# Performance work log

Hardware: AMD Instinct MI355X
Metric: run time of the kernel (lower is better)

Reference implementation:

```python
import jax, jax.numpy as jnp
import numpy as np

D_IN = 1024
D_OUT = 1024
NUM_HEADS = 16
HEAD_DIM = D_OUT // NUM_HEADS


def setup_inputs() -> dict:
    key = jax.random.key(0)
    kx, kq, kk, kv, ko = jax.random.split(key, 5)
    s = 1.0 / np.sqrt(D_IN)
    return {
        "x": jax.random.normal(kx, (1, 4096, D_IN), dtype=jnp.float32),
        "Wq": jax.random.normal(kq, (D_IN, D_OUT), dtype=jnp.float32) * s,
        "Wk": jax.random.normal(kk, (D_IN, D_OUT), dtype=jnp.float32) * s,
        "Wv": jax.random.normal(kv, (D_IN, D_OUT), dtype=jnp.float32) * s,
        "Wo": jax.random.normal(ko, (D_OUT, D_OUT), dtype=jnp.float32) * s,
    }


def reference(x, Wq, Wk, Wv, Wo):
    b, s, _ = x.shape
    # project and split heads: [b, h, s, d]
    def split_heads(t):
        return t.reshape(b, s, NUM_HEADS, HEAD_DIM).transpose(0, 2, 1, 3)
    Q = split_heads(x @ Wq)
    K = split_heads(x @ Wk)
    V = split_heads(x @ Wv)
    scores = jnp.einsum("bhqd,bhkd->bhqk", Q, K) / jnp.sqrt(jnp.float32(HEAD_DIM))
    causal = jnp.triu(jnp.ones((s, s), dtype=bool), k=1)  # True above diagonal
    scores = jnp.where(causal, -jnp.inf, scores)
    probs = jax.nn.softmax(scores, axis=-1)
    out = jnp.einsum("bhqk,bhkd->bhqd", probs, V)
    out = out.transpose(0, 2, 1, 3).reshape(b, s, D_OUT)
    return out @ Wo
```

## Files before the change

kernel.cpp:

```cpp
#include <hip/hip_runtime.h>
#include <cstdint>

#define S_LEN 4096
#define D_MODEL 1024
#define NHEAD 16
#define HDIM 64

typedef __bf16 bf16_t;
typedef __bf16 bf16x8 __attribute__((ext_vector_type(8)));
typedef __bf16 bf16x4 __attribute__((ext_vector_type(4)));
typedef float floatx4 __attribute__((ext_vector_type(4)));

#define QSCALE 0.18033688011112042f

__device__ __forceinline__ void lds_cp16(void* lds, const void* g) {
    __builtin_amdgcn_global_load_lds(
        (const __attribute__((address_space(1))) unsigned int*)g,
        (__attribute__((address_space(3))) unsigned int*)lds,
        16, 0, 0);
}

__device__ __forceinline__ float fast_exp2(float x) {
    float r;
    asm("v_exp_f32 %0, %1" : "=v"(r) : "v"(x));
    return r;
}

__global__ __launch_bounds__(256) void k_prep(const float* __restrict__ x,
                                              const float* __restrict__ Wq,
                                              const float* __restrict__ Wk,
                                              const float* __restrict__ Wv,
                                              const float* __restrict__ Wo,
                                              bf16_t* __restrict__ xb,
                                              bf16_t* __restrict__ WtQKV,
                                              bf16_t* __restrict__ WtO) {
    const int bx = blockIdx.x;
    if (bx < 4096) {
        int i = bx * 256 + threadIdx.x;
        float4 v = ((const float4*)x)[i];
        bf16x4 o;
        o[0] = (bf16_t)v.x; o[1] = (bf16_t)v.y; o[2] = (bf16_t)v.z; o[3] = (bf16_t)v.w;
        *(bf16x4*)(xb + (size_t)i * 4) = o;
        return;
    }
    __shared__ float lds[64][65];
    const int i = bx - 4096;
    const int z = i >> 8, rem = i & 255;
    const float* W = (z == 0) ? Wq : (z == 1) ? Wk : (z == 2) ? Wv : Wo;
    bf16_t* Wt = (z < 3) ? (WtQKV + (size_t)z * 1048576) : WtO;
    const int k0 = (rem >> 4) * 64, n0 = (rem & 15) * 64;
    const int t = threadIdx.x, cl = t & 63, rl = t >> 6;
#pragma unroll
    for (int r = 0; r < 16; ++r)
        lds[r * 4 + rl][cl] = W[(size_t)(k0 + r * 4 + rl) * 1024 + n0 + cl];
    __syncthreads();
#pragma unroll
    for (int r = 0; r < 16; ++r)
        Wt[(size_t)(n0 + r * 4 + rl) * 1024 + k0 + cl] = (bf16_t)lds[cl][r * 4 + rl];
}

template <int MODE, int MT>
__global__ __launch_bounds__(256) void k_gemm(const bf16_t* __restrict__ A,
                                              const bf16_t* __restrict__ Bt,
                                              float* __restrict__ Cout,
                                              bf16_t* __restrict__ Qb,
                                              bf16_t* __restrict__ Kb,
                                              bf16_t* __restrict__ Vt,
                                              const bf16_t* __restrict__ OP1x,
                                              const float* __restrict__ Lpx) {
    constexpr int MI = MT / 32;
    constexpr int GX = 4096 / MT;
    constexpr int GY = (MODE == 1) ? 24 : 8;
    constexpr int NWG = GX * GY;
    __shared__ __align__(16) bf16_t sA[MT * 32];
    __shared__ __align__(16) bf16_t sB[128 * 32];
    const int t = threadIdx.x, w = t >> 6, lane = t & 63, quad = lane >> 4, l15 = lane & 15;
    int lin = (int)blockIdx.y * GX + (int)blockIdx.x;
    lin = (lin & 7) * (NWG / 8) + (lin >> 3);
    const int bxr = lin % GX, byr = lin / GX;
    const int m0 = bxr * MT, n0 = byr * 128;
    const int wm = w >> 1, wn = w & 1;

    floatx4 acc[MI][4];
#pragma unroll
    for (int i = 0; i < MI; ++i)
#pragma unroll
        for (int j = 0; j < 4; ++j)
            acc[i][j] = floatx4{0.f, 0.f, 0.f, 0.f};

    const int crow = m0 + (t >> 2), ckq = t & 3;
    bf16x8 cA{}, cB{};
    float cla = 0.f, clb = 0.f;
    if (MODE == 2) {
        cA = *(const bf16x8*)(A + (size_t)crow * 1024 + ckq * 8);
        cB = *(const bf16x8*)(OP1x + (size_t)crow * 1024 + ckq * 8);
        cla = Lpx[crow];
        clb = Lpx[65536 + crow];
    }

    for (int kb = 0; kb < 32; ++kb) {
        __syncthreads();
        if (MODE == 2) {
            float inv = __builtin_amdgcn_rcpf(cla + clb);
            bf16x8 o;
#pragma unroll
            for (int e = 0; e < 8; ++e)
                o[e] = (bf16_t)(((float)cA[e] + (float)cB[e]) * inv);
            *(bf16x8*)&sA[t * 8] = o;
            if (kb + 1 < 32) {
                int h2 = (kb + 1) >> 1;
                int col = (kb + 1) * 32 + ckq * 8;
                cA = *(const bf16x8*)(A + (size_t)crow * 1024 + col);
                cB = *(const bf16x8*)(OP1x + (size_t)crow * 1024 + col);
                cla = Lpx[h2 * 4096 + crow];
                clb = Lpx[65536 + h2 * 4096 + crow];
            }
        } else {
#pragma unroll
            for (int r = 0; r < MT / 64; ++r) {
                int c = t + 256 * r;
                int row = c >> 2, kq = c & 3;
                lds_cp16(&sA[w * 512 + r * 2048],
                         A + (size_t)(m0 + row) * 1024 + kb * 32 + kq * 8);
            }
        }
#pragma unroll
        for (int r = 0; r < 2; ++r) {
            int c = t + 256 * r;
            int row = c >> 2, kq = c & 3;
            lds_cp16(&sB[w * 512 + r * 2048],
                     Bt + (size_t)(n0 + row) * 1024 + kb * 32 + kq * 8);
        }
        __syncthreads();
        bf16x8 af[MI], bfr[4];
#pragma unroll
        for (int i = 0; i < MI; ++i)
            af[i] = *(const bf16x8*)&sA[(wm * (MT / 2) + i * 16 + l15) * 32 + quad * 8];
#pragma unroll
        for (int j = 0; j < 4; ++j)
            bfr[j] = *(const bf16x8*)&sB[(wn * 64 + j * 16 + l15) * 32 + quad * 8];
#pragma unroll
        for (int i = 0; i < MI; ++i)
#pragma unroll
            for (int j = 0; j < 4; ++j)
                acc[i][j] = __builtin_amdgcn_mfma_f32_16x16x32_bf16(af[i], bfr[j],
                                                                    acc[i][j], 0, 0, 0);
    }

    const int mrow = m0 + wm * (MT / 2) + quad * 4;
    if (MODE == 0 || MODE == 2) {
        const int ncol = n0 + wn * 64 + l15;
#pragma unroll
        for (int i = 0; i < MI; ++i)
#pragma unroll
            for (int j = 0; j < 4; ++j)
#pragma unroll
                for (int r = 0; r < 4; ++r)
                    Cout[(size_t)(mrow + i * 16 + r) * 1024 + ncol + j * 16] = acc[i][j][r];
    } else {
        const int g = byr >> 3;
        const int ncbase = (byr & 7) * 128 + wn * 64 + l15;
        if (g == 2) {
#pragma unroll
            for (int j = 0; j < 4; ++j) {
                int nc = ncbase + j * 16;
                int hh = nc >> 6, dd = nc & 63;
                bf16_t* dst = Vt + (size_t)hh * 262144 + (size_t)dd * 64;
#pragma unroll
                for (int i = 0; i < MI; ++i) {
                    int s0r = mrow + i * 16;
                    bf16x4 pk;
                    pk[0] = (bf16_t)acc[i][j][0]; pk[1] = (bf16_t)acc[i][j][1];
                    pk[2] = (bf16_t)acc[i][j][2]; pk[3] = (bf16_t)acc[i][j][3];
                    int kk = s0r & 63;
                    int pp = (kk & 0x20) | ((kk & 0xC) << 1) | ((kk & 0x10) >> 2);
                    *(bf16x4*)&dst[(size_t)(s0r >> 6) * 4096 + pp] = pk;
                }
            }
        } else {
            bf16_t* base = g ? Kb : Qb;
            const float sc = g ? 1.0f : QSCALE;
#pragma unroll
            for (int j = 0; j < 4; ++j) {
                int nc = ncbase + j * 16;
                int hh = nc >> 6, dd = nc & 63;
#pragma unroll
                for (int i = 0; i < MI; ++i)
#pragma unroll
                    for (int r = 0; r < 4; ++r)
                        base[(size_t)hh * 262144 + (size_t)(mrow + i * 16 + r) * 64 + dd] =
                            (bf16_t)(acc[i][j][r] * sc);
            }
        }
    }
}

__global__ __launch_bounds__(256, 4) void k_attn(const bf16_t* __restrict__ Qb,
                                                 const bf16_t* __restrict__ Kb,
                                                 const bf16_t* __restrict__ Vt,
                                                 bf16_t* __restrict__ OP0,
                                                 bf16_t* __restrict__ OP1,
                                                 float* __restrict__ Lp) {
    __shared__ __align__(16) bf16_t Ks[2][64 * 64];
    __shared__ __align__(16) bf16_t Vts[2][64 * 64];
    const int bid = blockIdx.x;
    const int slot = bid >> 8, jj = bid & 255, g = jj >> 5, u = jj & 31;
    const int h = u >> 1, sp = u & 1;
    const int qb = (slot == 0) ? (31 - g) : (slot == 1) ? (16 + g)
                 : (slot == 2) ? (15 - g) : g;
    const int t = threadIdx.x, w = t >> 6, quad = (t & 63) >> 4, l15 = t & 15;
    const bf16_t* Qh = Qb + (size_t)h * 262144;
    const bf16_t* Kh = Kb + (size_t)h * 262144;
    const bf16_t* Vth = Vt + (size_t)h * 262144;

    const bf16_t* Qrow = Qh + (size_t)(qb * 128 + w * 32 + l15) * 64;
    bf16x8 bq[2][2];
#pragma unroll
    for (int qt = 0; qt < 2; ++qt)
#pragma unroll
        for (int kh = 0; kh < 2; ++kh)
            bq[qt][kh] = *(const bf16x8*)(Qrow + qt * 1024 + kh * 32 + quad * 8);

    bf16x8 vones;
#pragma unroll
    for (int e = 0; e < 8; ++e) vones[e] = (bf16_t)1.0f;

    floatx4 lacc[2];
    floatx4 o_acc[2][4];
#pragma unroll
    for (int qt = 0; qt < 2; ++qt) {
        lacc[qt] = floatx4{0.f, 0.f, 0.f, 0.f};
#pragma unroll
        for (int j = 0; j < 4; ++j) o_acc[qt][j] = floatx4{0.f, 0.f, 0.f, 0.f};
    }

#define STAGE_K(b, kb_)                                                            \
    {                                                                              \
        _Pragma("unroll") for (int r = 0; r < 2; ++r) {                            \
            int c = t + 256 * r;                                                   \
            int row = c >> 3, sw = (c & 7) ^ (row & 7);                            \
            lds_cp16(&Ks[b][c * 8], Kh + (size_t)(kb_) * 4096 + row * 64 + sw * 8);\
        }                                                                          \
    }
#define STAGE_V(b, kb_)                                                            \
    {                                                                              \
        _Pragma("unroll") for (int r = 0; r < 2; ++r) {                            \
            int c = t + 256 * r;                                                   \
            int row = c >> 3, sw = (c & 7) ^ (row & 7);                            \
            lds_cp16(&Vts[b][c * 8], Vth + (size_t)(kb_) * 4096 + row * 64 + sw * 8);\
        }                                                                          \
    }

    const int t0 = sp ? (qb + 1) : 0;
    const int nIter = qb + 1;
    const int qmax = qb * 128 + w * 32 + 31;

    STAGE_K(0, t0)
    STAGE_V(0, t0)
    for (int it = 0; it < nIter; ++it) {
        const int kb = t0 + it;
        const int buf = it & 1;
        __syncthreads();
        if (it + 1 < nIter) {
            STAGE_K(buf ^ 1, kb + 1)
            STAGE_V(buf ^ 1, kb + 1)
        }
        const bool active = (kb * 64 <= qmax);

        if (active) {
            floatx4 st[2][4];
            __builtin_amdgcn_s_setprio(1);
#pragma unroll
            for (int j = 0; j < 4; ++j) {
                int rk = j * 16 + l15;
                bf16x8 a0 = *(const bf16x8*)&Ks[buf][rk * 64 + ((quad ^ (rk & 7)) * 8)];
                bf16x8 a1 = *(const bf16x8*)&Ks[buf][rk * 64 + (((quad + 4) ^ (rk & 7)) * 8)];
#pragma unroll
                for (int qt = 0; qt < 2; ++qt) {
                    floatx4 z = {0.f, 0.f, 0.f, 0.f};
                    st[qt][j] = __builtin_amdgcn_mfma_f32_16x16x32_bf16(a0, bq[qt][0], z, 0, 0, 0);
                    st[qt][j] = __builtin_amdgcn_mfma_f32_16x16x32_bf16(a1, bq[qt][1], st[qt][j], 0, 0, 0);
                }
            }
            __builtin_amdgcn_s_setprio(0);
            if (kb >= 2 * qb) {
#pragma unroll
                for (int qt = 0; qt < 2; ++qt) {
                    int qg = qb * 128 + w * 32 + qt * 16 + l15;
#pragma unroll
                    for (int j = 0; j < 4; ++j)
#pragma unroll
                        for (int r = 0; r < 4; ++r) {
                            int keyg = kb * 64 + j * 16 + quad * 4 + r;
                            if (keyg > qg) st[qt][j][r] = -1e30f;
                        }
                }
            }
            bf16x8 pa[2][2];
#pragma unroll
            for (int qt = 0; qt < 2; ++qt) {
#pragma unroll
                for (int j = 0; j < 4; ++j) {
                    st[qt][j][0] = fast_exp2(st[qt][j][0]);
                    st[qt][j][1] = fast_exp2(st[qt][j][1]);
                    st[qt][j][2] = fast_exp2(st[qt][j][2]);
                    st[qt][j][3] = fast_exp2(st[qt][j][3]);
                }
#pragma unroll
                for (int kh = 0; kh < 2; ++kh)
#pragma unroll
                    for (int m = 0; m < 4; ++m) {
                        pa[qt][kh][m]     = (bf16_t)st[qt][2 * kh][m];
                        pa[qt][kh][4 + m] = (bf16_t)st[qt][2 * kh + 1][m];
                    }
            }
            __builtin_amdgcn_s_setprio(1);
#pragma unroll
            for (int kh = 0; kh < 2; ++kh) {
                int pc = kh * 4 + quad;
#pragma unroll
                for (int j = 0; j < 4; ++j) {
                    int rd = j * 16 + l15;
                    bf16x8 bv = *(const bf16x8*)&Vts[buf][rd * 64 + ((pc ^ (rd & 7)) * 8)];
                    o_acc[0][j] = __builtin_amdgcn_mfma_f32_16x16x32_bf16(pa[0][kh], bv, o_acc[0][j], 0, 0, 0);
                    o_acc[1][j] = __builtin_amdgcn_mfma_f32_16x16x32_bf16(pa[1][kh], bv, o_acc[1][j], 0, 0, 0);
                }
                lacc[0] = __builtin_amdgcn_mfma_f32_16x16x32_bf16(pa[0][kh], vones, lacc[0], 0, 0, 0);
                lacc[1] = __builtin_amdgcn_mfma_f32_16x16x32_bf16(pa[1][kh], vones, lacc[1], 0, 0, 0);
            }
            __builtin_amdgcn_s_setprio(0);
        }
    }
    bf16_t* OPx = sp ? OP1 : OP0;
#pragma unroll
    for (int qt = 0; qt < 2; ++qt) {
        if (l15 == 0)
            *(floatx4*)&Lp[sp * 65536 + h * 4096 + qb * 128 + w * 32 + qt * 16 + quad * 4] =
                lacc[qt];
#pragma unroll
        for (int r = 0; r < 4; ++r) {
            int rowg = qb * 128 + w * 32 + qt * 16 + quad * 4 + r;
#pragma unroll
            for (int j = 0; j < 4; ++j)
                OPx[(size_t)rowg * 1024 + h * 64 + j * 16 + l15] = (bf16_t)o_acc[qt][j][r];
        }
    }
#undef STAGE_K
#undef STAGE_V
}

extern "C" void kernel_launch(void* const* d_in, const int* in_sizes, int n_in,
                              void* d_out, int out_size, void* d_ws, size_t ws_size,
                              hipStream_t stream) {
    const float* x  = (const float*)d_in[0];
    const float* Wq = (const float*)d_in[1];
    const float* Wk = (const float*)d_in[2];
    const float* Wv = (const float*)d_in[3];
    const float* Wo = (const float*)d_in[4];

    bf16_t* ws = (bf16_t*)d_ws;
    bf16_t* Xb    = ws;
    bf16_t* WtQKV = Xb + 4194304;
    bf16_t* WtO   = WtQKV + 3145728;
    bf16_t* Qb    = WtO + 1048576;
    bf16_t* Kb    = Qb + 4194304;
    bf16_t* Vt    = Kb + 4194304;
    bf16_t* OP1   = Vt + 4194304;
    bf16_t* OP0   = Xb;
    float*  Lp    = (float*)WtQKV;
    float* out = (float*)d_out;

    k_prep<<<5120, 256, 0, stream>>>(x, Wq, Wk, Wv, Wo, Xb, WtQKV, WtO);
    k_gemm<1, 128><<<dim3(32, 24), 256, 0, stream>>>(Xb, WtQKV, nullptr, Qb, Kb, Vt,
                                                     nullptr, nullptr);
    k_attn<<<1024, 256, 0, stream>>>(Qb, Kb, Vt, OP0, OP1, Lp);
    k_gemm<2, 64><<<dim3(64, 8), 256, 0, stream>>>(OP0, WtO, out, nullptr, nullptr,
                                                   nullptr, OP1, Lp);
}
```

Before: 192.8 us.

## Use persistent atomic work queue with 3-way KV split for long attention rows

The attention kernel becomes persistent. Each block grabs chunks from a global atomic counter that is zeroed in the prep kernel and stored in the output buffer. The upper half of query blocks now splits the KV range three ways instead of two, with a third partial output buffer OP2. The output GEMM merges three partial sums for those rows. The aim is better load balance on the causal triangle; the cost is atomic overhead, extra partial-output traffic, and removal of the GEMM block-swizzle remapping.

```diff
diff --git a/kernel.cpp b/kernel.cpp
--- a/kernel.cpp
+++ b/kernel.cpp
@@ -12,6 +12,7 @@
 typedef float floatx4 __attribute__((ext_vector_type(4)));
 
 #define QSCALE 0.18033688011112042f
+#define NCHUNK 1280
 
 __device__ __forceinline__ void lds_cp16(void* lds, const void* g) {
     __builtin_amdgcn_global_load_lds(
@@ -33,7 +34,8 @@
                                               const float* __restrict__ Wo,
                                               bf16_t* __restrict__ xb,
                                               bf16_t* __restrict__ WtQKV,
-                                              bf16_t* __restrict__ WtO) {
+                                              bf16_t* __restrict__ WtO,
+                                              unsigned int* __restrict__ ctr) {
     const int bx = blockIdx.x;
     if (bx < 4096) {
         int i = bx * 256 + threadIdx.x;
@@ -43,6 +45,7 @@
         *(bf16x4*)(xb + (size_t)i * 4) = o;
         return;
     }
+    if (bx == 4096 && threadIdx.x == 0) *ctr = 0u;
     __shared__ float lds[64][65];
     const int i = bx - 4096;
     const int z = i >> 8, rem = i & 255;
@@ -67,18 +70,13 @@
                                               bf16_t* __restrict__ Kb,
                                               bf16_t* __restrict__ Vt,
                                               const bf16_t* __restrict__ OP1x,
+                                              const bf16_t* __restrict__ OP2x,
                                               const float* __restrict__ Lpx) {
     constexpr int MI = MT / 32;
-    constexpr int GX = 4096 / MT;
-    constexpr int GY = (MODE == 1) ? 24 : 8;
-    constexpr int NWG = GX * GY;
     __shared__ __align__(16) bf16_t sA[MT * 32];
     __shared__ __align__(16) bf16_t sB[128 * 32];
     const int t = threadIdx.x, w = t >> 6, lane = t & 63, quad = lane >> 4, l15 = lane & 15;
-    int lin = (int)blockIdx.y * GX + (int)blockIdx.x;
-    lin = (lin & 7) * (NWG / 8) + (lin >> 3);
-    const int bxr = lin % GX, byr = lin / GX;
-    const int m0 = bxr * MT, n0 = byr * 128;
+    const int m0 = blockIdx.x * MT, n0 = blockIdx.y * 128;
     const int wm = w >> 1, wn = w & 1;
 
     floatx4 acc[MI][4];
@@ -89,23 +87,28 @@
             acc[i][j] = floatx4{0.f, 0.f, 0.f, 0.f};
 
     const int crow = m0 + (t >> 2), ckq = t & 3;
-    bf16x8 cA{}, cB{};
-    float cla = 0.f, clb = 0.f;
+    const bool hasC = (MODE == 2) && (crow >= 2048);
+    bf16x8 cA{}, cB{}, cC{};
+    float cla = 0.f, clb = 0.f, clc = 0.f;
     if (MODE == 2) {
         cA = *(const bf16x8*)(A + (size_t)crow * 1024 + ckq * 8);
         cB = *(const bf16x8*)(OP1x + (size_t)crow * 1024 + ckq * 8);
         cla = Lpx[crow];
         clb = Lpx[65536 + crow];
+        if (hasC) {
+            cC = *(const bf16x8*)(OP2x + (size_t)(crow - 2048) * 1024 + ckq * 8);
+            clc = Lpx[131072 + crow];
+        }
     }
 
     for (int kb = 0; kb < 32; ++kb) {
         __syncthreads();
         if (MODE == 2) {
-            float inv = __builtin_amdgcn_rcpf(cla + clb);
+            float inv = __builtin_amdgcn_rcpf(cla + clb + clc);
             bf16x8 o;
 #pragma unroll
             for (int e = 0; e < 8; ++e)
-                o[e] = (bf16_t)(((float)cA[e] + (float)cB[e]) * inv);
+                o[e] = (bf16_t)(((float)cA[e] + (float)cB[e] + (float)cC[e]) * inv);
             *(bf16x8*)&sA[t * 8] = o;
             if (kb + 1 < 32) {
                 int h2 = (kb + 1) >> 1;
@@ -114,6 +117,10 @@
                 cB = *(const bf16x8*)(OP1x + (size_t)crow * 1024 + col);
                 cla = Lpx[h2 * 4096 + crow];
                 clb = Lpx[65536 + h2 * 4096 + crow];
+                if (hasC) {
+                    cC = *(const bf16x8*)(OP2x + (size_t)(crow - 2048) * 1024 + col);
+                    clc = Lpx[131072 + h2 * 4096 + crow];
+                }
             }
         } else {
 #pragma unroll
@@ -158,8 +165,8 @@
                 for (int r = 0; r < 4; ++r)
                     Cout[(size_t)(mrow + i * 16 + r) * 1024 + ncol + j * 16] = acc[i][j][r];
     } else {
-        const int g = byr >> 3;
-        const int ncbase = (byr & 7) * 128 + wn * 64 + l15;
+        const int g = (int)blockIdx.y >> 3;
+        const int ncbase = ((int)blockIdx.y & 7) * 128 + wn * 64 + l15;
         if (g == 2) {
 #pragma unroll
             for (int j = 0; j < 4; ++j) {
@@ -200,39 +207,17 @@
                                                  const bf16_t* __restrict__ Vt,
                                                  bf16_t* __restrict__ OP0,
                                                  bf16_t* __restrict__ OP1,
-                                                 float* __restrict__ Lp) {
+                                                 bf16_t* __restrict__ OP2,
+                                                 float* __restrict__ Lp,
+                                                 unsigned int* __restrict__ ctr) {
     __shared__ __align__(16) bf16_t Ks[2][64 * 64];
     __shared__ __align__(16) bf16_t Vts[2][64 * 64];
-    const int bid = blockIdx.x;
-    const int slot = bid >> 8, jj = bid & 255, g = jj >> 5, u = jj & 31;
-    const int h = u >> 1, sp = u & 1;
-    const int qb = (slot == 0) ? (31 - g) : (slot == 1) ? (16 + g)
-                 : (slot == 2) ? (15 - g) : g;
+    __shared__ int sid;
     const int t = threadIdx.x, w = t >> 6, quad = (t & 63) >> 4, l15 = t & 15;
-    const bf16_t* Qh = Qb + (size_t)h * 262144;
-    const bf16_t* Kh = Kb + (size_t)h * 262144;
-    const bf16_t* Vth = Vt + (size_t)h * 262144;
-
-    const bf16_t* Qrow = Qh + (size_t)(qb * 128 + w * 32 + l15) * 64;
-    bf16x8 bq[2][2];
-#pragma unroll
-    for (int qt = 0; qt < 2; ++qt)
-#pragma unroll
-        for (int kh = 0; kh < 2; ++kh)
-            bq[qt][kh] = *(const bf16x8*)(Qrow + qt * 1024 + kh * 32 + quad * 8);
 
     bf16x8 vones;
 #pragma unroll
     for (int e = 0; e < 8; ++e) vones[e] = (bf16_t)1.0f;
-
-    floatx4 lacc[2];
-    floatx4 o_acc[2][4];
-#pragma unroll
-    for (int qt = 0; qt < 2; ++qt) {
-        lacc[qt] = floatx4{0.f, 0.f, 0.f, 0.f};
-#pragma unroll
-        for (int j = 0; j < 4; ++j) o_acc[qt][j] = floatx4{0.f, 0.f, 0.f, 0.f};
-    }
 
 #define STAGE_K(b, kb_)                                                            \
     {                                                                              \
@@ -251,98 +236,144 @@
         }                                                                          \
     }
 
-    const int t0 = sp ? (qb + 1) : 0;
-    const int nIter = qb + 1;
-    const int qmax = qb * 128 + w * 32 + 31;
-
-    STAGE_K(0, t0)
-    STAGE_V(0, t0)
-    for (int it = 0; it < nIter; ++it) {
-        const int kb = t0 + it;
-        const int buf = it & 1;
+    for (;;) {
+        if (t == 0) sid = (int)atomicAdd(ctr, 1u);
         __syncthreads();
-        if (it + 1 < nIter) {
-            STAGE_K(buf ^ 1, kb + 1)
-            STAGE_V(buf ^ 1, kb + 1)
-        }
-        const bool active = (kb * 64 <= qmax);
-
-        if (active) {
-            floatx4 st[2][4];
-            __builtin_amdgcn_s_setprio(1);
-#pragma unroll
-            for (int j = 0; j < 4; ++j) {
-                int rk = j * 16 + l15;
-                bf16x8 a0 = *(const bf16x8*)&Ks[buf][rk * 64 + ((quad ^ (rk & 7)) * 8)];
-                bf16x8 a1 = *(const bf16x8*)&Ks[buf][rk * 64 + (((quad + 4) ^ (rk & 7)) * 8)];
+        const int id = sid;
+        if (id >= NCHUNK) break;
+
+        int qb, h, part, c0, c1;
+        if (id < 768) {
+            qb = 31 - id / 48;
+            int r = id % 48;
+            h = r / 3; part = r % 3;
+            int L = 2 * qb + 2, base = L / 3, rem = L % 3;
+            int mn = part < rem ? part : rem;
+            c0 = part * base + mn;
+            c1 = c0 + base + (part < rem ? 1 : 0);
+        } else {
+            int j = id - 768;
+            qb = 15 - (j >> 5);
+            int r = j & 31;
+            h = r >> 1; part = r & 1;
+            c0 = part ? (qb + 1) : 0;
+            c1 = part ? (2 * qb + 2) : (qb + 1);
+        }
+        const bf16_t* Qh = Qb + (size_t)h * 262144;
+        const bf16_t* Kh = Kb + (size_t)h * 262144;
+        const bf16_t* Vth = Vt + (size_t)h * 262144;
+
+        const bf16_t* Qrow = Qh + (size_t)(qb * 128 + w * 32 + l15) * 64;
+        bf16x8 bq[2][2];
+#pragma unroll
+        for (int qt = 0; qt < 2; ++qt)
+#pragma unroll
+            for (int kh = 0; kh < 2; ++kh)
+                bq[qt][kh] = *(const bf16x8*)(Qrow + qt * 1024 + kh * 32 + quad * 8);
+
+        floatx4 lacc[2];
+        floatx4 o_acc[2][4];
+#pragma unroll
+        for (int qt = 0; qt < 2; ++qt) {
+            lacc[qt] = floatx4{0.f, 0.f, 0.f, 0.f};
+#pragma unroll
+            for (int j = 0; j < 4; ++j) o_acc[qt][j] = floatx4{0.f, 0.f, 0.f, 0.f};
+        }
+
+        const int nIter = c1 - c0;
+        const int qmax = qb * 128 + w * 32 + 31;
+
+        STAGE_K(0, c0)
+        STAGE_V(0, c0)
+        for (int it = 0; it < nIter; ++it) {
+            const int kb = c0 + it;
+            const int buf = it & 1;
+            __syncthreads();
+            if (it + 1 < nIter) {
+                STAGE_K(buf ^ 1, kb + 1)
+                STAGE_V(buf ^ 1, kb + 1)
+            }
+            const bool active = (kb * 64 <= qmax);
+
+            if (active) {
+                floatx4 st[2][4];
+                __builtin_amdgcn_s_setprio(1);
+#pragma unroll
+                for (int j = 0; j < 4; ++j) {
+                    int rk = j * 16 + l15;
+                    bf16x8 a0 = *(const bf16x8*)&Ks[buf][rk * 64 + ((quad ^ (rk & 7)) * 8)];
+                    bf16x8 a1 = *(const bf16x8*)&Ks[buf][rk * 64 + (((quad + 4) ^ (rk & 7)) * 8)];
+#pragma unroll
+                    for (int qt = 0; qt < 2; ++qt) {
+                        floatx4 z = {0.f, 0.f, 0.f, 0.f};
+                        st[qt][j] = __builtin_amdgcn_mfma_f32_16x16x32_bf16(a0, bq[qt][0], z, 0, 0, 0);
+                        st[qt][j] = __builtin_amdgcn_mfma_f32_16x16x32_bf16(a1, bq[qt][1], st[qt][j], 0, 0, 0);
+                    }
+                }
+                __builtin_amdgcn_s_setprio(0);
+                if (kb >= 2 * qb) {
+#pragma unroll
+                    for (int qt = 0; qt < 2; ++qt) {
+                        int qg = qb * 128 + w * 32 + qt * 16 + l15;
+#pragma unroll
+                        for (int j = 0; j < 4; ++j)
+#pragma unroll
+                            for (int r = 0; r < 4; ++r) {
+                                int keyg = kb * 64 + j * 16 + quad * 4 + r;
+                                if (keyg > qg) st[qt][j][r] = -1e30f;
+                            }
+                    }
+                }
+                bf16x8 pa[2][2];
 #pragma unroll
                 for (int qt = 0; qt < 2; ++qt) {
-                    floatx4 z = {0.f, 0.f, 0.f, 0.f};
-                    st[qt][j] = __builtin_amdgcn_mfma_f32_16x16x32_bf16(a0, bq[qt][0], z, 0, 0, 0);
-                    st[qt][j] = __builtin_amdgcn_mfma_f32_16x16x32_bf16(a1, bq[qt][1], st[qt][j], 0, 0, 0);
-                }
-            }
-            __builtin_amdgcn_s_setprio(0);
-            if (kb >= 2 * qb) {
-#pragma unroll
-                for (int qt = 0; qt < 2; ++qt) {
-                    int qg = qb * 128 + w * 32 + qt * 16 + l15;
-#pragma unroll
-                    for (int j = 0; j < 4; ++j)
-#pragma unroll
-                        for (int r = 0; r < 4; ++r) {
-                            int keyg = kb * 64 + j * 16 + quad * 4 + r;
-                            if (keyg > qg) st[qt][j][r] = -1e30f;
+#pragma unroll
+                    for (int j = 0; j < 4; ++j) {
+                        st[qt][j][0] = fast_exp2(st[qt][j][0]);
+                        st[qt][j][1] = fast_exp2(st[qt][j][1]);
+                        st[qt][j][2] = fast_exp2(st[qt][j][2]);
+                        st[qt][j][3] = fast_exp2(st[qt][j][3]);
+                    }
+#pragma unroll
+                    for (int kh = 0; kh < 2; ++kh)
+#pragma unroll
+                        for (int m = 0; m < 4; ++m) {
+                            pa[qt][kh][m]     = (bf16_t)st[qt][2 * kh][m];
+                            pa[qt][kh][4 + m] = (bf16_t)st[qt][2 * kh + 1][m];
                         }
                 }
-            }
-            bf16x8 pa[2][2];
-#pragma unroll
-            for (int qt = 0; qt < 2; ++qt) {
-#pragma unroll
-                for (int j = 0; j < 4; ++j) {
-                    st[qt][j][0] = fast_exp2(st[qt][j][0]);
-                    st[qt][j][1] = fast_exp2(st[qt][j][1]);
-                    st[qt][j][2] = fast_exp2(st[qt][j][2]);
-                    st[qt][j][3] = fast_exp2(st[qt][j][3]);
-                }
-#pragma unroll
-                for (int kh = 0; kh < 2; ++kh)
-#pragma unroll
-                    for (int m = 0; m < 4; ++m) {
-                        pa[qt][kh][m]     = (bf16_t)st[qt][2 * kh][m];
-                        pa[qt][kh][4 + m] = (bf16_t)st[qt][2 * kh + 1][m];
+                __builtin_amdgcn_s_setprio(1);
+#pragma unroll
+                for (int kh = 0; kh < 2; ++kh) {
+                    int pc = kh * 4 + quad;
+#pragma unroll
+                    for (int j = 0; j < 4; ++j) {
+                        int rd = j * 16 + l15;
+                        bf16x8 bv = *(const bf16x8*)&Vts[buf][rd * 64 + ((pc ^ (rd & 7)) * 8)];
+                        o_acc[0][j] = __builtin_amdgcn_mfma_f32_16x16x32_bf16(pa[0][kh], bv, o_acc[0][j], 0, 0, 0);
+                        o_acc[1][j] = __builtin_amdgcn_mfma_f32_16x16x32_bf16(pa[1][kh], bv, o_acc[1][j], 0, 0, 0);
                     }
-            }
-            __builtin_amdgcn_s_setprio(1);
-#pragma unroll
-            for (int kh = 0; kh < 2; ++kh) {
-                int pc = kh * 4 + quad;
-#pragma unroll
-                for (int j = 0; j < 4; ++j) {
-                    int rd = j * 16 + l15;
-                    bf16x8 bv = *(const bf16x8*)&Vts[buf][rd * 64 + ((pc ^ (rd & 7)) * 8)];
-                    o_acc[0][j] = __builtin_amdgcn_mfma_f32_16x16x32_bf16(pa[0][kh], bv, o_acc[0][j], 0, 0, 0);
-                    o_acc[1][j] = __builtin_amdgcn_mfma_f32_16x16x32_bf16(pa[1][kh], bv, o_acc[1][j], 0, 0, 0);
-                }
-                lacc[0] = __builtin_amdgcn_mfma_f32_16x16x32_bf16(pa[0][kh], vones, lacc[0], 0, 0, 0);
-                lacc[1] = __builtin_amdgcn_mfma_f32_16x16x32_bf16(pa[1][kh], vones, lacc[1], 0, 0, 0);
-            }
-            __builtin_amdgcn_s_setprio(0);
-        }
-    }
-    bf16_t* OPx = sp ? OP1 : OP0;
-#pragma unroll
-    for (int qt = 0; qt < 2; ++qt) {
-        if (l15 == 0)
-            *(floatx4*)&Lp[sp * 65536 + h * 4096 + qb * 128 + w * 32 + qt * 16 + quad * 4] =
-                lacc[qt];
-#pragma unroll
-        for (int r = 0; r < 4; ++r) {
-            int rowg = qb * 128 + w * 32 + qt * 16 + quad * 4 + r;
-#pragma unroll
-            for (int j = 0; j < 4; ++j)
-                OPx[(size_t)rowg * 1024 + h * 64 + j * 16 + l15] = (bf16_t)o_acc[qt][j][r];
+                    lacc[0] = __builtin_amdgcn_mfma_f32_16x16x32_bf16(pa[0][kh], vones, lacc[0], 0, 0, 0);
+                    lacc[1] = __builtin_amdgcn_mfma_f32_16x16x32_bf16(pa[1][kh], vones, lacc[1], 0, 0, 0);
+                }
+                __builtin_amdgcn_s_setprio(0);
+            }
+        }
+        bf16_t* OPx = (part == 0) ? OP0 : (part == 1) ? OP1 : OP2;
+        const int rsub = (part == 2) ? 2048 : 0;
+#pragma unroll
+        for (int qt = 0; qt < 2; ++qt) {
+            if (l15 == 0)
+                *(floatx4*)&Lp[part * 65536 + h * 4096 + qb * 128 + w * 32 + qt * 16 + quad * 4] =
+                    lacc[qt];
+#pragma unroll
+            for (int r = 0; r < 4; ++r) {
+                int rowg = qb * 128 + w * 32 + qt * 16 + quad * 4 + r;
+#pragma unroll
+                for (int j = 0; j < 4; ++j)
+                    OPx[(size_t)(rowg - rsub) * 1024 + h * 64 + j * 16 + l15] =
+                        (bf16_t)o_acc[qt][j][r];
+            }
         }
     }
 #undef STAGE_K
@@ -368,12 +399,14 @@
     bf16_t* OP1   = Vt + 4194304;
     bf16_t* OP0   = Xb;
     float*  Lp    = (float*)WtQKV;
+    bf16_t* OP2   = WtQKV + 393216;
     float* out = (float*)d_out;
-
-    k_prep<<<5120, 256, 0, stream>>>(x, Wq, Wk, Wv, Wo, Xb, WtQKV, WtO);
+    unsigned int* ctr = (unsigned int*)d_out;
+
+    k_prep<<<5120, 256, 0, stream>>>(x, Wq, Wk, Wv, Wo, Xb, WtQKV, WtO, ctr);
     k_gemm<1, 128><<<dim3(32, 24), 256, 0, stream>>>(Xb, WtQKV, nullptr, Qb, Kb, Vt,
-                                                     nullptr, nullptr);
-    k_attn<<<1024, 256, 0, stream>>>(Qb, Kb, Vt, OP0, OP1, Lp);
+                                                     nullptr, nullptr, nullptr);
+    k_attn<<<1024, 256, 0, stream>>>(Qb, Kb, Vt, OP0, OP1, OP2, Lp, ctr);
     k_gemm<2, 64><<<dim3(64, 8), 256, 0, stream>>>(OP0, WtO, out, nullptr, nullptr,
-                                                   nullptr, OP1, Lp);
-}
+                                                   nullptr, OP1, OP2, Lp);
+}
```

After: 198.3 us. +2.8%, slower.
